# Kernel optimization log

Hardware: AMD Instinct MI355X
Metric: run time of the kernel (lower is better)

The kernel has to match this reference:

```python
import jax, jax.numpy as jnp
import numpy as np

N_NODES = 50000
DIM = 64
HEADS = 4
N_EDGES = 800000
NEG_SLOPE = 0.2  # PyG GATConv default


def setup_inputs() -> dict:
    key = jax.random.key(0)
    ks = jax.random.split(key, 8)
    H, C = HEADS, DIM
    embedding = jax.random.normal(ks[0], (N_NODES, DIM), dtype=jnp.float32)
    graph = jax.random.randint(ks[1], (2, N_EDGES), 0, N_NODES, dtype=jnp.int64)
    s = 1.0 / np.sqrt(DIM)
    # GATConv params: shared source/target linear (PyG uses one lin when in_channels is int)
    W = jax.random.normal(ks[2], (DIM, H * C), dtype=jnp.float32) * s
    att_src = jax.random.normal(ks[3], (H, C), dtype=jnp.float32) * s
    att_dst = jax.random.normal(ks[4], (H, C), dtype=jnp.float32) * s
    bias = jnp.zeros((H * C,), dtype=jnp.float32)
    # dense: Linear(dim*heads -> dim)
    dense_w = jax.random.normal(ks[5], (H * C, DIM), dtype=jnp.float32) / np.sqrt(H * C)
    dense_b = jnp.zeros((DIM,), dtype=jnp.float32)
    return {"embedding": embedding, "graph": graph, "W": W, "att_src": att_src,
            "att_dst": att_dst, "bias": bias, "dense_w": dense_w, "dense_b": dense_b}


def reference(embedding, graph, W, att_src, att_dst, bias, dense_w, dense_b):
    N, D = embedding.shape
    H, C = att_src.shape
    # linear projection, per-head view: [N, H, C]
    x = (embedding @ W).reshape(N, H, C)
    # add self loops (PyG default add_self_loops=True)
    ar = jnp.arange(N, dtype=graph.dtype)
    src = jnp.concatenate([graph[0], ar])  # [E+N]
    dst = jnp.concatenate([graph[1], ar])
    # per-node attention logits, gathered per edge
    a_src = jnp.einsum('nhc,hc->nh', x, att_src)  # [N, H]
    a_dst = jnp.einsum('nhc,hc->nh', x, att_dst)
    alpha = jax.nn.leaky_relu(a_src[src] + a_dst[dst], NEG_SLOPE)  # [E, H]
    # segment softmax over destination nodes
    amax = jax.ops.segment_max(alpha, dst, num_segments=N)  # [N, H]
    amax = jnp.where(jnp.isfinite(amax), amax, 0.0)
    ex = jnp.exp(alpha - amax[dst])
    denom = jax.ops.segment_sum(ex, dst, num_segments=N)
    coef = ex / (denom[dst] + 1e-16)  # [E, H]
    # weighted scatter-aggregate of source features
    msg = x[src] * coef[:, :, None]  # [E, H, C]
    agg = jax.ops.segment_sum(msg, dst, num_segments=N)  # [N, H, C]
    gat_out = agg.reshape(N, H * C) + bias  # concat heads + bias
    return gat_out @ dense_w + dense_b  # [N, D]
```

## Files before the change

### kernel.cpp

```cpp
#include <hip/hip_runtime.h>
#include <hip/hip_fp16.h>
#include <cfloat>
#include <cmath>

#define DIM 64
#define HEADS 4
#define NEG 0.2f
#define CAP 64

__device__ __forceinline__ float lrelu(float a) { return a > 0.0f ? a : NEG * a; }

__device__ __forceinline__ unsigned pack_half2(float a, float b) {
    return (unsigned)__half_as_ushort(__float2half(a)) |
           ((unsigned)__half_as_ushort(__float2half(b)) << 16);
}

__global__ __launch_bounds__(256) void prep_kernel(
        const float* __restrict__ W, const float* __restrict__ dw,
        const float* __restrict__ att_s, const float* __restrict__ att_d,
        const float* __restrict__ bias, const float* __restrict__ db,
        const float* __restrict__ emb,
        float* __restrict__ M, float* __restrict__ bvec,
        float* __restrict__ a_src, float* __restrict__ a_dst,
        int* __restrict__ cnt, int N) {
    const int b = blockIdx.x, t = threadIdx.x;
    if (b < 64) {
        __shared__ float s_W[256];
        s_W[t] = W[b * 256 + t];
        __syncthreads();
        const int h = t >> 6, j = t & 63;
        float s = 0.f;
        for (int c = 0; c < 64; c++)
            s = fmaf(s_W[h * 64 + c], dw[(h * 64 + c) * 64 + j], s);
        M[b * 256 + t] = s;
    } else if (b == 64) {
        __shared__ float s_p[256];
        const int j = t & 63, kq = t >> 6;
        float p = 0.f;
        for (int k = kq * 64; k < kq * 64 + 64; k++)
            p = fmaf(bias[k], dw[k * 64 + j], p);
        s_p[t] = p;
        __syncthreads();
        if (t < 64)
            bvec[t] = s_p[t] + s_p[64 + t] + s_p[128 + t] + s_p[192 + t] + db[t];
    } else {
        __shared__ float s_e[64 * 68];
        __shared__ float s_vs[256], s_vd[256];
        const int n0 = (b - 65) * 64;
        {
            const int d = t >> 2, h = t & 3;
            const float4* w4 = (const float4*)(W + d * 256 + h * 64);
            const float4* s4 = (const float4*)(att_s + h * 64);
            const float4* d4 = (const float4*)(att_d + h * 64);
            float vs = 0.f, vd = 0.f;
#pragma unroll
            for (int k = 0; k < 16; k++) {
                float4 w = w4[k], as = s4[k], ad = d4[k];
                vs = fmaf(w.x, as.x, fmaf(w.y, as.y, fmaf(w.z, as.z, fmaf(w.w, as.w, vs))));
                vd = fmaf(w.x, ad.x, fmaf(w.y, ad.y, fmaf(w.z, ad.z, fmaf(w.w, ad.w, vd))));
            }
            s_vs[h * 64 + d] = vs;
            s_vd[h * 64 + d] = vd;
        }
#pragma unroll
        for (int r = 0; r < 4; r++) {
            int idx = (r * 256 + t) * 4;
            int i = idx >> 6, d = idx & 63;
            int row = min(n0 + i, N - 1);
            *(float4*)(s_e + i * 68 + d) = *(const float4*)(emb + (size_t)row * 64 + d);
        }
        __syncthreads();
        const int node = t >> 2, h = t & 3;
        const float* er = s_e + node * 68;
        float as = 0.f, ad = 0.f;
#pragma unroll
        for (int g = 0; g < 16; g++) {
            float4 ev = *(const float4*)(er + 4 * g);
            float4 vs = *(const float4*)(s_vs + h * 64 + 4 * g);
            float4 vd = *(const float4*)(s_vd + h * 64 + 4 * g);
            as = fmaf(ev.x, vs.x, fmaf(ev.y, vs.y, fmaf(ev.z, vs.z, fmaf(ev.w, vs.w, as))));
            ad = fmaf(ev.x, vd.x, fmaf(ev.y, vd.y, fmaf(ev.z, vd.z, fmaf(ev.w, vd.w, ad))));
        }
        const int n = n0 + node;
        if (n < N) {
            a_src[(size_t)n * 4 + h] = as;
            a_dst[(size_t)n * 4 + h] = ad;
        }
        if (t < 64 && n0 + t < N) cnt[n0 + t] = 0;
    }
}

__global__ __launch_bounds__(256) void mid_kernel(
        const int* __restrict__ gsrc, const int* __restrict__ gdst,
        int* __restrict__ cnt, int* __restrict__ adj,
        const float* __restrict__ emb, const float* __restrict__ M,
        unsigned* __restrict__ y32, int E, int N, int FB) {
    __shared__ float s_e[64 * 68];
    const int t = threadIdx.x;

    if ((int)blockIdx.x < FB) {
        const int e0 = (blockIdx.x * 256 + t) * 4;
        if (e0 >= E) return;
        if (e0 + 3 < E) {
            const int4 s4 = *(const int4*)(gsrc + e0);
            const int4 d4 = *(const int4*)(gdst + e0);
            const int p0 = atomicAdd(&cnt[d4.x], 1);
            const int p1 = atomicAdd(&cnt[d4.y], 1);
            const int p2 = atomicAdd(&cnt[d4.z], 1);
            const int p3 = atomicAdd(&cnt[d4.w], 1);
            if (p0 < CAP) adj[(size_t)d4.x * CAP + p0] = s4.x;
            if (p1 < CAP) adj[(size_t)d4.y * CAP + p1] = s4.y;
            if (p2 < CAP) adj[(size_t)d4.z * CAP + p2] = s4.z;
            if (p3 < CAP) adj[(size_t)d4.w * CAP + p3] = s4.w;
        } else {
            for (int e = e0; e < E; e++) {
                const int s = gsrc[e], dn = gdst[e];
                const int pos = atomicAdd(&cnt[dn], 1);
                if (pos < CAP) adj[(size_t)dn * CAP + pos] = s;
            }
        }
        return;
    }

    const int l = t & 63;
    const int wq = __builtin_amdgcn_readfirstlane(t >> 6);
    const int n0 = (blockIdx.x - FB) * 64;

#pragma unroll
    for (int r = 0; r < 4; r++) {
        int idx = (r * 256 + t) * 4;
        int i = idx >> 6, d = idx & 63;
        int row = min(n0 + i, N - 1);
        *(float4*)(s_e + i * 68 + d) = *(const float4*)(emb + (size_t)row * 64 + d);
    }
    __syncthreads();

    float4 acc[16];
#pragma unroll
    for (int i = 0; i < 16; i++) acc[i] = make_float4(0.f, 0.f, 0.f, 0.f);

    const float* eb = s_e + wq * 16 * 68;

    for (int g = 0; g < 16; g++) {
        const int d0 = g * 4;
        float4 wv0 = *(const float4*)(M + (d0 + 0) * 256 + 4 * l);
        float4 wv1 = *(const float4*)(M + (d0 + 1) * 256 + 4 * l);
        float4 wv2 = *(const float4*)(M + (d0 + 2) * 256 + 4 * l);
        float4 wv3 = *(const float4*)(M + (d0 + 3) * 256 + 4 * l);
#pragma unroll
        for (int i = 0; i < 16; i++) {
            float4 ev = *(const float4*)(eb + i * 68 + d0);
            acc[i].x = fmaf(ev.x, wv0.x, acc[i].x);
            acc[i].y = fmaf(ev.x, wv0.y, acc[i].y);
            acc[i].z = fmaf(ev.x, wv0.z, acc[i].z);
            acc[i].w = fmaf(ev.x, wv0.w, acc[i].w);
            acc[i].x = fmaf(ev.y, wv1.x, acc[i].x);
            acc[i].y = fmaf(ev.y, wv1.y, acc[i].y);
            acc[i].z = fmaf(ev.y, wv1.z, acc[i].z);
            acc[i].w = fmaf(ev.y, wv1.w, acc[i].w);
            acc[i].x = fmaf(ev.z, wv2.x, acc[i].x);
            acc[i].y = fmaf(ev.z, wv2.y, acc[i].y);
            acc[i].z = fmaf(ev.z, wv2.z, acc[i].z);
            acc[i].w = fmaf(ev.z, wv2.w, acc[i].w);
            acc[i].x = fmaf(ev.w, wv3.x, acc[i].x);
            acc[i].y = fmaf(ev.w, wv3.y, acc[i].y);
            acc[i].z = fmaf(ev.w, wv3.z, acc[i].z);
            acc[i].w = fmaf(ev.w, wv3.w, acc[i].w);
        }
    }

#pragma unroll
    for (int i = 0; i < 16; i++) {
        int n = n0 + wq * 16 + i;
        if (n < N) {
            uint2 u;
            u.x = pack_half2(acc[i].x, acc[i].y);
            u.y = pack_half2(acc[i].z, acc[i].w);
            *(uint2*)(y32 + (size_t)n * 128 + 2 * l) = u;
        }
    }
}

__global__ __launch_bounds__(256) void aggregate_kernel(
        const int* __restrict__ cnt, const int* __restrict__ adj,
        const float* __restrict__ a_src, const float* __restrict__ a_dst,
        const unsigned* __restrict__ y32, const float* __restrict__ bvec,
        float* __restrict__ out, int N) {
    const int t = threadIdx.x;
    const int l = t & 63;
    const int dd = blockIdx.x * 4 + (t >> 6);
    if (dd >= N) return;
    const int d = __builtin_amdgcn_readfirstlane(dd);
    const int hl = l >> 4;
    const int lh = l & 48;
    const int deg = min(__builtin_amdgcn_readfirstlane(cnt[d]), CAP);
    const unsigned* yl = y32 + 2 * l;

    int my_src = 0;
    if (l < deg) my_src = adj[(size_t)d * CAP + l];

    const float ad = a_dst[(size_t)d * 4 + hl];

    float pv0, pv1, pv2, pv3;
    {
        const int q = l & 15;
#define PRE_PV(G, PV) {                                                    \
            const int e_ = (G) * 16 + q;                                   \
            const int se_ = __shfl(my_src, e_, 64);                        \
            float pe_ = 0.f;                                               \
            if (e_ < deg)                                                  \
                pe_ = __expf(lrelu(a_src[(size_t)se_ * 4 + hl] + ad));     \
            (PV) = pe_; }
        PRE_PV(0, pv0); PRE_PV(1, pv1); PRE_PV(2, pv2); PRE_PV(3, pv3);
#undef PRE_PV
    }

    float den, ax, ay, az, aw;
    {
        const float p = __expf(lrelu(a_src[(size_t)d * 4 + hl] + ad));
        const uint2 v = *(const uint2*)(yl + (size_t)d * 128);
        const float2 f0 = __half22float2(*(const __half2*)&v.x);
        const float2 f1 = __half22float2(*(const __half2*)&v.y);
        den = p;
        ax = p * f0.x; ay = p * f0.y; az = p * f1.x; aw = p * f1.y;
    }

#define AGG_EDGE(PG, I, J) {                                               \
        const int si_ = __builtin_amdgcn_readlane(my_src, (I));            \
        const float pe_ = __shfl((PG), lh + (J), 64);                      \
        const uint2 vv_ = *(const uint2*)(yl + (size_t)si_ * 128);         \
        const float2 g0_ = __half22float2(*(const __half2*)&vv_.x);        \
        const float2 g1_ = __half22float2(*(const __half2*)&vv_.y);        \
        den += pe_;                                                        \
        ax = fmaf(pe_, g0_.x, ax); ay = fmaf(pe_, g0_.y, ay);              \
        az = fmaf(pe_, g1_.x, az); aw = fmaf(pe_, g1_.y, aw); }

#define AGG_GROUP(G, PG) {                                                 \
        const int base_ = (G) * 16;                                        \
        if (base_ < deg) {                                                 \
            const int mp_ = min(16, ((deg - base_) + 3) & ~3);             \
            _Pragma("unroll 1")                                            \
            for (int j = 0; j < mp_; j += 4) {                             \
                AGG_EDGE(PG, base_ + j + 0, j + 0);                        \
                AGG_EDGE(PG, base_ + j + 1, j + 1);                        \
                AGG_EDGE(PG, base_ + j + 2, j + 2);                        \
                AGG_EDGE(PG, base_ + j + 3, j + 3);                        \
            }                                                              \
        } }

    AGG_GROUP(0, pv0);
    AGG_GROUP(1, pv1);
    AGG_GROUP(2, pv2);
    AGG_GROUP(3, pv3);
#undef AGG_GROUP
#undef AGG_EDGE

    const float inv = 1.0f / (den + 1e-16f);
    float rx = ax * inv, ry = ay * inv, rz = az * inv, rw = aw * inv;
    rx += __shfl_xor(rx, 16, 64); ry += __shfl_xor(ry, 16, 64);
    rz += __shfl_xor(rz, 16, 64); rw += __shfl_xor(rw, 16, 64);
    rx += __shfl_xor(rx, 32, 64); ry += __shfl_xor(ry, 32, 64);
    rz += __shfl_xor(rz, 32, 64); rw += __shfl_xor(rw, 32, 64);
    if (l < 16) {
        float4 bv = *(const float4*)(bvec + 4 * l);
        float4 r;
        r.x = rx + bv.x; r.y = ry + bv.y; r.z = rz + bv.z; r.w = rw + bv.w;
        *(float4*)(out + (size_t)dd * 64 + 4 * l) = r;
    }
}

extern "C" void kernel_launch(void* const* d_in, const int* in_sizes, int n_in,
                              void* d_out, int out_size, void* d_ws, size_t ws_size,
                              hipStream_t stream) {
    const float* emb   = (const float*)d_in[0];
    const int*   graph = (const int*)d_in[1];
    const float* W     = (const float*)d_in[2];
    const float* att_s = (const float*)d_in[3];
    const float* att_d = (const float*)d_in[4];
    const float* bias  = (const float*)d_in[5];
    const float* dw    = (const float*)d_in[6];
    const float* db    = (const float*)d_in[7];
    float* out = (float*)d_out;

    const int N = in_sizes[0] / DIM;
    const int E = in_sizes[1] / 2;
    const int* gsrc = graph;
    const int* gdst = graph + E;

    unsigned* y32  = (unsigned*)d_ws;
    int* adj       = (int*)(y32 + (size_t)N * 128);
    float* a_src   = (float*)(adj + (size_t)N * CAP);
    float* a_dst   = a_src + (size_t)N * 4;
    float* M       = a_dst + (size_t)N * 4;
    float* bvec    = M + 64 * 256;
    int*   cnt     = (int*)(bvec + 64);

    const int quads = (E + 3) / 4;
    const int FB = (quads + 255) / 256;
    const int PB = (N + 63) / 64;

    hipLaunchKernelGGL(prep_kernel, dim3(65 + PB), dim3(256), 0, stream,
                       W, dw, att_s, att_d, bias, db, emb,
                       M, bvec, a_src, a_dst, cnt, N);
    hipLaunchKernelGGL(mid_kernel, dim3(FB + PB), dim3(256), 0, stream,
                       gsrc, gdst, cnt, adj, emb, M, y32, E, N, FB);
    hipLaunchKernelGGL(aggregate_kernel, dim3((N + 3) / 4), dim3(256), 0, stream,
                       cnt, adj, a_src, a_dst, y32, bvec, out, N);
}
```

Before: 221.9 us.

## Partition edge-bucketing by destination range across block groups for L2 locality

The adjacency fill now splits destination nodes into 8 ranges, with 96 blocks per range. Each block scans all edges but only performs atomics and adj writes for destinations in its own range. This confines the atomic and scatter traffic to a smaller slice of the cnt and adj arrays (likely within one XCD's L2), at the cost of reading the edge list 8 times. Edge loads and the half-precision y stores also switch to nontemporal hints.

```diff
diff --git a/kernel.cpp b/kernel.cpp
--- a/kernel.cpp
+++ b/kernel.cpp
@@ -7,6 +7,10 @@
 #define HEADS 4
 #define NEG 0.2f
 #define CAP 64
+#define NPART 8
+#define BPP 96
+
+typedef int v4i __attribute__((ext_vector_type(4)));
 
 __device__ __forceinline__ float lrelu(float a) { return a > 0.0f ? a : NEG * a; }
 
@@ -99,24 +103,35 @@
     const int t = threadIdx.x;
 
     if ((int)blockIdx.x < FB) {
-        const int e0 = (blockIdx.x * 256 + t) * 4;
-        if (e0 >= E) return;
-        if (e0 + 3 < E) {
-            const int4 s4 = *(const int4*)(gsrc + e0);
-            const int4 d4 = *(const int4*)(gdst + e0);
-            const int p0 = atomicAdd(&cnt[d4.x], 1);
-            const int p1 = atomicAdd(&cnt[d4.y], 1);
-            const int p2 = atomicAdd(&cnt[d4.z], 1);
-            const int p3 = atomicAdd(&cnt[d4.w], 1);
-            if (p0 < CAP) adj[(size_t)d4.x * CAP + p0] = s4.x;
-            if (p1 < CAP) adj[(size_t)d4.y * CAP + p1] = s4.y;
-            if (p2 < CAP) adj[(size_t)d4.z * CAP + p2] = s4.z;
-            if (p3 < CAP) adj[(size_t)d4.w * CAP + p3] = s4.w;
-        } else {
-            for (int e = e0; e < E; e++) {
-                const int s = gsrc[e], dn = gdst[e];
-                const int pos = atomicAdd(&cnt[dn], 1);
-                if (pos < CAP) adj[(size_t)dn * CAP + pos] = s;
+        const int part = blockIdx.x & (NPART - 1);
+        const int slot = blockIdx.x >> 3;
+        const int lo = (int)((long long)part * N / NPART);
+        const int hi = (int)((long long)(part + 1) * N / NPART);
+        const unsigned span = (unsigned)(hi - lo);
+        const int quads = (E + 3) >> 2;
+        const int stride = BPP * 256;
+
+        for (int q = slot * 256 + t; q < quads; q += stride) {
+            const int e0 = q * 4;
+            v4i s4, d4;
+            if (e0 + 3 < E) {
+                d4 = __builtin_nontemporal_load((const v4i*)(gdst + e0));
+                s4 = __builtin_nontemporal_load((const v4i*)(gsrc + e0));
+            } else {
+#pragma unroll
+                for (int k = 0; k < 4; k++) {
+                    const int e = e0 + k;
+                    d4[k] = (e < E) ? gdst[e] : -1;
+                    s4[k] = (e < E) ? gsrc[e] : 0;
+                }
+            }
+#pragma unroll
+            for (int k = 0; k < 4; k++) {
+                const int d = d4[k];
+                if ((unsigned)(d - lo) < span) {
+                    const int pos = atomicAdd(&cnt[d], 1);
+                    if (pos < CAP) adj[(size_t)d * CAP + pos] = s4[k];
+                }
             }
         }
         return;
@@ -173,10 +188,11 @@
     for (int i = 0; i < 16; i++) {
         int n = n0 + wq * 16 + i;
         if (n < N) {
-            uint2 u;
-            u.x = pack_half2(acc[i].x, acc[i].y);
-            u.y = pack_half2(acc[i].z, acc[i].w);
-            *(uint2*)(y32 + (size_t)n * 128 + 2 * l) = u;
+            unsigned long long u =
+                (unsigned long long)pack_half2(acc[i].x, acc[i].y) |
+                ((unsigned long long)pack_half2(acc[i].z, acc[i].w) << 32);
+            __builtin_nontemporal_store(u,
+                (unsigned long long*)(y32 + (size_t)n * 128 + 2 * l));
         }
     }
 }
@@ -295,15 +311,14 @@
     float* bvec    = M + 64 * 256;
     int*   cnt     = (int*)(bvec + 64);
 
-    const int quads = (E + 3) / 4;
-    const int FB = (quads + 255) / 256;
+    const int FILLB = NPART * BPP;
     const int PB = (N + 63) / 64;
 
     hipLaunchKernelGGL(prep_kernel, dim3(65 + PB), dim3(256), 0, stream,
                        W, dw, att_s, att_d, bias, db, emb,
                        M, bvec, a_src, a_dst, cnt, N);
-    hipLaunchKernelGGL(mid_kernel, dim3(FB + PB), dim3(256), 0, stream,
-                       gsrc, gdst, cnt, adj, emb, M, y32, E, N, FB);
+    hipLaunchKernelGGL(mid_kernel, dim3(FILLB + PB), dim3(256), 0, stream,
+                       gsrc, gdst, cnt, adj, emb, M, y32, E, N, FILLB);
     hipLaunchKernelGGL(aggregate_kernel, dim3((N + 3) / 4), dim3(256), 0, stream,
                        cnt, adj, a_src, a_dst, y32, bvec, out, N);
 }
```

New measurement: 220.7 us. Within noise of the previous version (-0.6%).
